# Kernel optimization log

Hardware: AMD Instinct MI355X
Metric: run time of the kernel (lower is better)

The kernel has to match this reference:

```python
import jax, jax.numpy as jnp
import numpy as np

B, LMAX, H, D = 128, 256, 16, 64
NEG_INF = -1e9  # finite mask value to keep padded softmax rows NaN-free


def _lengths():
    # deterministic varlen mix: 64 seqs of 128 tokens, 64 of 256 -> total 24576
    lens = np.array([128] * 64 + [256] * 64, dtype=np.int64)
    rng = np.random.default_rng(0)
    rng.shuffle(lens)
    return lens


def setup_inputs() -> dict:
    key = jax.random.key(0)
    lens = _lengths()
    cu = np.zeros(B + 1, dtype=np.int64)
    cu[1:] = np.cumsum(lens)
    T = int(cu[-1])  # 24576 packed tokens

    kq, kk, kv = jax.random.split(key, 3)
    q = jax.random.normal(kq, (T, H, D), dtype=jnp.float32)
    k = jax.random.normal(kk, (T, H, D), dtype=jnp.float32)
    v = jax.random.normal(kv, (T, H, D), dtype=jnp.float32)

    pos = np.arange(LMAX)[None, :]                      # [1, LMAX]
    mask = pos < lens[:, None]                          # [B, LMAX] valid-token mask
    gather_idx = np.where(mask, cu[:-1, None] + pos, 0).astype(np.int32)

    # packed token t -> flat padded index b*LMAX + (t - cu[b])
    b_of = np.repeat(np.arange(B), lens)
    inv_idx = (b_of * LMAX + (np.arange(T) - cu[b_of])).astype(np.int32)

    return {
        "q": q, "k": k, "v": v,
        "cu_seqlens_q": jnp.asarray(cu, dtype=jnp.int32),
        "cu_seqlens_k": jnp.asarray(cu, dtype=jnp.int32),
        "gather_idx": jnp.asarray(gather_idx),
        "mask": jnp.asarray(mask),
        "inv_idx": jnp.asarray(inv_idx),
        "max_seqlen_q": LMAX,
        "max_seqlen_k": LMAX,
    }


def reference(q, k, v, cu_seqlens_q, cu_seqlens_k, gather_idx, mask, inv_idx,
              max_seqlen_q, max_seqlen_k):
    # Pad packed [T,H,D] -> [B,L,H,D]; padded slots point at token 0 but are masked out.
    qp = q[gather_idx]  # [B, L, H, D]
    kp = k[gather_idx]
    vp = v[gather_idx]
    scale = 1.0 / jnp.sqrt(jnp.asarray(q.shape[-1], q.dtype))
    scores = jnp.einsum("bqhd,bkhd->bhqk", qp, kp) * scale  # [B, H, L, L]
    scores = jnp.where(mask[:, None, None, :], scores, NEG_INF)
    w = jax.nn.softmax(scores, axis=-1)
    out_p = jnp.einsum("bhqk,bkhd->bqhd", w, vp)            # [B, L, H, D]
    # Unpad back to packed layout [T, H, D]
    return out_p.reshape(-1, q.shape[1], q.shape[2])[inv_idx]
```

## Files before the change

kernel.cpp:

```cpp
#include <hip/hip_runtime.h>
#include <hip/hip_bf16.h>


using bf16x8 = __attribute__((ext_vector_type(8))) short;
using u16x8  = __attribute__((ext_vector_type(8))) unsigned short;
using f32x4  = __attribute__((ext_vector_type(4))) float;

#define MFMA(a, b, c) __builtin_amdgcn_mfma_f32_16x16x32_bf16((a), (b), (c), 0, 0, 0)

constexpr int H  = 16;
constexpr int D  = 64;
constexpr int RS = H * D;
constexpr float QSCALE = 0.125f * 1.44269504088896f;
constexpr float THR    = 11.5f;

__device__ inline unsigned short bfbits(float x) {
  return __builtin_bit_cast(unsigned short, __float2bfloat16(x));
}
__device__ inline float bff(unsigned short u) {
  unsigned v = ((unsigned)u) << 16;
  return __builtin_bit_cast(float, v);
}

__global__ __launch_bounds__(512, 4)
void fa_mfma4_kernel(const float* __restrict__ qg, const float* __restrict__ kg,
                     const float* __restrict__ vg, const int* __restrict__ cu,
                     float* __restrict__ outg) {
  __shared__ unsigned short kph[2][64 * 64];
  __shared__ unsigned short kpl[2][64 * 64];
  __shared__ unsigned short vth[2][64 * 64];

  const int bid   = (int)blockIdx.x;
  const int pp    = ((bid >> 4) << 3) + (bid & 7);
  const int chunk = (bid >> 3) & 1;
  const int b = pp >> 4, h = pp & 15;

  const int t0 = cu[b];
  const int L  = cu[b + 1] - t0;
  if (chunk * 128 >= L) return;
  const int nt = L >> 6;

  const int tid = (int)threadIdx.x, lane = tid & 63, w = tid >> 6;
  const int g = lane >> 4, qj = lane & 15;

  const int s_key = tid >> 3, s_d0 = (tid & 7) * 8;
  const int kidx  = s_key * 64 + (((s_d0 >> 3) ^ (s_key & 7)) << 3);
  const int s_vd  = tid & 63,  s_k0 = (tid >> 6) * 8;
  const int vidx  = s_vd * 64 + (((s_k0 >> 3) ^ (s_vd & 7)) << 3);

  const float* kbase = kg + (size_t)t0 * RS + h * D;
  const float* vbase = vg + (size_t)t0 * RS + h * D;

  bf16x8 qh[2], ql[2];
  {
    const float* qrow = qg + (size_t)(t0 + chunk * 128 + w * 16 + qj) * RS + h * D;
#pragma unroll
    for (int ks = 0; ks < 2; ++ks) {
      const float4 f0 = *reinterpret_cast<const float4*>(qrow + ks * 32 + g * 8);
      const float4 f1 = *reinterpret_cast<const float4*>(qrow + ks * 32 + g * 8 + 4);
      const float f[8] = {f0.x, f0.y, f0.z, f0.w, f1.x, f1.y, f1.z, f1.w};
#pragma unroll
      for (int j = 0; j < 8; ++j) {
        const float x = f[j] * QSCALE;
        const unsigned short hs = bfbits(x);
        qh[ks][j] = (short)hs;
        ql[ks][j] = (short)bfbits(x - bff(hs));
      }
    }
  }

  f32x4 acc[4];
#pragma unroll
  for (int n = 0; n < 4; ++n) acc[n] = (f32x4){0.f, 0.f, 0.f, 0.f};
  float m = -1e30f, lsum = 0.f;

  float4 ka, kb; float va[8];
  auto load_t = [&](int t) {
    const float* kr = kbase + (size_t)(t * 64 + s_key) * RS + s_d0;
    ka = *reinterpret_cast<const float4*>(kr);
    kb = *reinterpret_cast<const float4*>(kr + 4);
    const float* vp = vbase + (size_t)(t * 64 + s_k0) * RS + s_vd;
#pragma unroll
    for (int i = 0; i < 8; ++i) va[i] = vp[(size_t)i * RS];
  };
  auto cvt_write = [&](int buf) {
    u16x8 ch, cl, cv;
    const float kf[8] = {ka.x, ka.y, ka.z, ka.w, kb.x, kb.y, kb.z, kb.w};
#pragma unroll
    for (int i = 0; i < 8; ++i) {
      const unsigned short hs = bfbits(kf[i]);
      ch[i] = hs;
      cl[i] = bfbits(kf[i] - bff(hs));
    }
#pragma unroll
    for (int i = 0; i < 8; ++i) cv[i] = bfbits(va[i]);
    *reinterpret_cast<u16x8*>(&kph[buf][kidx]) = ch;
    *reinterpret_cast<u16x8*>(&kpl[buf][kidx]) = cl;
    *reinterpret_cast<u16x8*>(&vth[buf][vidx]) = cv;
  };

  auto compute = [&](int buf) {
    const unsigned short* KH = kph[buf];
    const unsigned short* KL = kpl[buf];
    const unsigned short* VT = vth[buf];
    f32x4 sc[4];
#pragma unroll
    for (int kt = 0; kt < 4; ++kt) sc[kt] = (f32x4){0.f, 0.f, 0.f, 0.f};
    __builtin_amdgcn_s_setprio(1);
#pragma unroll
    for (int kt = 0; kt < 4; ++kt) {
#pragma unroll
      for (int ks = 0; ks < 2; ++ks) {
        const int idx = (kt * 16 + qj) * 64 + (((ks * 4 + g) ^ (qj & 7)) << 3);
        const bf16x8 khi = *reinterpret_cast<const bf16x8*>(&KH[idx]);
        const bf16x8 klo = *reinterpret_cast<const bf16x8*>(&KL[idx]);
        sc[kt] = MFMA(khi, qh[ks], sc[kt]);
        sc[kt] = MFMA(klo, qh[ks], sc[kt]);
        sc[kt] = MFMA(khi, ql[ks], sc[kt]);
      }
    }
    __builtin_amdgcn_s_setprio(0);

    float tmax = sc[0][0];
#pragma unroll
    for (int kt = 0; kt < 4; ++kt)
#pragma unroll
      for (int r = 0; r < 4; ++r) tmax = fmaxf(tmax, sc[kt][r]);
    tmax = fmaxf(tmax, __shfl_xor(tmax, 16));
    tmax = fmaxf(tmax, __shfl_xor(tmax, 32));
    if (!__all(tmax <= m + THR)) {
      const float newm = fmaxf(m, tmax);
      const float corr = exp2f(m - newm);
      m = newm;
      lsum *= corr;
#pragma unroll
      for (int r = 0; r < 4; ++r) {
        const float cr = __shfl(corr, g * 4 + r);
#pragma unroll
        for (int n = 0; n < 4; ++n) acc[n][r] *= cr;
      }
    }
    float p[4][4], ps = 0.f;
#pragma unroll
    for (int kt = 0; kt < 4; ++kt)
#pragma unroll
      for (int r = 0; r < 4; ++r) {
        p[kt][r] = exp2f(sc[kt][r] - m);
        ps += p[kt][r];
      }
    ps += __shfl_xor(ps, 16);
    ps += __shfl_xor(ps, 32);
    lsum += ps;

#pragma unroll
    for (int c = 0; c < 2; ++c) {
      bf16x8 pah, pal;
#pragma unroll
      for (int j = 0; j < 8; ++j) {
        const int sl  = (((2 * g + (j >> 2)) & 3) << 4) + qj;
        const float fa = __shfl(p[2 * c][j & 3], sl);
        const float fb = __shfl(p[2 * c + 1][j & 3], sl);
        const float pv = (g & 2) ? fb : fa;
        const unsigned short hb = bfbits(pv);
        pah[j] = (short)hb;
        pal[j] = (short)bfbits(pv - bff(hb));
      }
      __builtin_amdgcn_s_setprio(1);
#pragma unroll
      for (int n = 0; n < 4; ++n) {
        const int idx = (n * 16 + qj) * 64 + (((4 * c + g) ^ (qj & 7)) << 3);
        const bf16x8 vh = *reinterpret_cast<const bf16x8*>(&VT[idx]);
        acc[n] = MFMA(pah, vh, acc[n]);
        acc[n] = MFMA(pal, vh, acc[n]);
      }
      __builtin_amdgcn_s_setprio(0);
    }
  };

  load_t(0);
  cvt_write(0);
  if (nt > 1) load_t(1);
  asm volatile("s_waitcnt lgkmcnt(0)" ::: "memory");
  __builtin_amdgcn_s_barrier();
  asm volatile("" ::: "memory");

  for (int t = 0; t < nt; ++t) {
    const int cur = t & 1;
    if (t + 1 < nt) {
      cvt_write(cur ^ 1);
      if (t + 2 < nt) load_t(t + 2);
    }
    compute(cur);
    if (t + 1 < nt) {
      asm volatile("s_waitcnt lgkmcnt(0)" ::: "memory");
      __builtin_amdgcn_s_barrier();
      asm volatile("" ::: "memory");
    }
  }

  const float linv = 1.0f / lsum;
#pragma unroll
  for (int r = 0; r < 4; ++r) {
    const float lr = __shfl(linv, g * 4 + r);
    const int qrow = chunk * 128 + w * 16 + g * 4 + r;
    float* op = outg + (size_t)(t0 + qrow) * RS + h * D + qj;
    op[0]  = acc[0][r] * lr;
    op[16] = acc[1][r] * lr;
    op[32] = acc[2][r] * lr;
    op[48] = acc[3][r] * lr;
  }
}

extern "C" void kernel_launch(void* const* d_in, const int* in_sizes, int n_in,
                              void* d_out, int out_size, void* d_ws, size_t ws_size,
                              hipStream_t stream) {
  (void)in_sizes; (void)n_in; (void)d_ws; (void)ws_size; (void)out_size;
  const float* q  = (const float*)d_in[0];
  const float* k  = (const float*)d_in[1];
  const float* v  = (const float*)d_in[2];
  const int*   cu = (const int*)d_in[3];
  float* out = (float*)d_out;

  fa_mfma4_kernel<<<dim3(4096), dim3(512), 0, stream>>>(q, k, v, cu, out);
}
```

Before: 124.4 us.

## Switch attention to 32x32x16 MFMA tiles with 4 waves per block

Replaces the 16x16x32 bf16 MFMA tiling with 32x32x16 MFMAs, so each wave owns 32 query rows and blocks shrink from 8 to 4 waves. The K/V staging loads now pull 16 elements per thread. The P-matrix repacking moves from many per-element shuffles to a half-wave xor exchange of packed bf16 pairs, and row-wise correction factors go through shared memory. The goal is fewer MFMA issues, less shuffle overhead and more reuse per LDS read, at the cost of more registers per thread and lower occupancy.

```diff
diff --git a/kernel.cpp b/kernel.cpp
--- a/kernel.cpp
+++ b/kernel.cpp
@@ -4,9 +4,10 @@
 
 using bf16x8 = __attribute__((ext_vector_type(8))) short;
 using u16x8  = __attribute__((ext_vector_type(8))) unsigned short;
-using f32x4  = __attribute__((ext_vector_type(4))) float;
-
-#define MFMA(a, b, c) __builtin_amdgcn_mfma_f32_16x16x32_bf16((a), (b), (c), 0, 0, 0)
+using u32x4  = __attribute__((ext_vector_type(4))) unsigned;
+using f32x16 = __attribute__((ext_vector_type(16))) float;
+
+#define MFMA32(a, b, c) __builtin_amdgcn_mfma_f32_32x32x16_bf16((a), (b), (c), 0, 0, 0)
 
 constexpr int H  = 16;
 constexpr int D  = 64;
@@ -21,14 +22,18 @@
   unsigned v = ((unsigned)u) << 16;
   return __builtin_bit_cast(float, v);
 }
-
-__global__ __launch_bounds__(512, 4)
-void fa_mfma4_kernel(const float* __restrict__ qg, const float* __restrict__ kg,
+__device__ inline unsigned pack2(float x, float y) {
+  return (unsigned)bfbits(x) | ((unsigned)bfbits(y) << 16);
+}
+
+__global__ __launch_bounds__(256, 3)
+void fa_mfma7_kernel(const float* __restrict__ qg, const float* __restrict__ kg,
                      const float* __restrict__ vg, const int* __restrict__ cu,
                      float* __restrict__ outg) {
   __shared__ unsigned short kph[2][64 * 64];
   __shared__ unsigned short kpl[2][64 * 64];
   __shared__ unsigned short vth[2][64 * 64];
+  __shared__ float lsc[4 * 32];
 
   const int bid   = (int)blockIdx.x;
   const int pp    = ((bid >> 4) << 3) + (bid & 7);
@@ -41,23 +46,27 @@
   const int nt = L >> 6;
 
   const int tid = (int)threadIdx.x, lane = tid & 63, w = tid >> 6;
-  const int g = lane >> 4, qj = lane & 15;
-
-  const int s_key = tid >> 3, s_d0 = (tid & 7) * 8;
-  const int kidx  = s_key * 64 + (((s_d0 >> 3) ^ (s_key & 7)) << 3);
-  const int s_vd  = tid & 63,  s_k0 = (tid >> 6) * 8;
-  const int vidx  = s_vd * 64 + (((s_k0 >> 3) ^ (s_vd & 7)) << 3);
+  const int hi = lane >> 5, qj = lane & 31;
+  const int qbase = chunk * 128 + w * 32;
+
+  const int k_key = tid >> 2, kd0 = (tid & 3) * 16;
+  const int kidx0 = k_key * 64 + ((((kd0 >> 3) + 0) ^ (k_key & 7)) << 3);
+  const int kidx1 = k_key * 64 + ((((kd0 >> 3) + 1) ^ (k_key & 7)) << 3);
+  const int v_d = tid & 63, vk0 = (tid >> 6) * 16;
+  const int vidx0 = v_d * 64 + ((((vk0 >> 3) + 0) ^ (v_d & 7)) << 3);
+  const int vidx1 = v_d * 64 + ((((vk0 >> 3) + 1) ^ (v_d & 7)) << 3);
 
   const float* kbase = kg + (size_t)t0 * RS + h * D;
   const float* vbase = vg + (size_t)t0 * RS + h * D;
 
-  bf16x8 qh[2], ql[2];
+  bf16x8 qh[4], ql[4];
   {
-    const float* qrow = qg + (size_t)(t0 + chunk * 128 + w * 16 + qj) * RS + h * D;
-#pragma unroll
-    for (int ks = 0; ks < 2; ++ks) {
-      const float4 f0 = *reinterpret_cast<const float4*>(qrow + ks * 32 + g * 8);
-      const float4 f1 = *reinterpret_cast<const float4*>(qrow + ks * 32 + g * 8 + 4);
+    const float* qrow = qg + (size_t)(t0 + qbase + qj) * RS + h * D;
+#pragma unroll
+    for (int ks = 0; ks < 4; ++ks) {
+      const int d0 = ks * 16 + hi * 8;
+      const float4 f0 = *reinterpret_cast<const float4*>(qrow + d0);
+      const float4 f1 = *reinterpret_cast<const float4*>(qrow + d0 + 4);
       const float f[8] = {f0.x, f0.y, f0.z, f0.w, f1.x, f1.y, f1.z, f1.w};
 #pragma unroll
       for (int j = 0; j < 8; ++j) {
@@ -69,109 +78,144 @@
     }
   }
 
-  f32x4 acc[4];
-#pragma unroll
-  for (int n = 0; n < 4; ++n) acc[n] = (f32x4){0.f, 0.f, 0.f, 0.f};
+  f32x16 acc0, acc1;
+#pragma unroll
+  for (int r = 0; r < 16; ++r) { acc0[r] = 0.f; acc1[r] = 0.f; }
   float m = -1e30f, lsum = 0.f;
 
-  float4 ka, kb; float va[8];
+  float kf[16], vf[16];
   auto load_t = [&](int t) {
-    const float* kr = kbase + (size_t)(t * 64 + s_key) * RS + s_d0;
-    ka = *reinterpret_cast<const float4*>(kr);
-    kb = *reinterpret_cast<const float4*>(kr + 4);
-    const float* vp = vbase + (size_t)(t * 64 + s_k0) * RS + s_vd;
-#pragma unroll
-    for (int i = 0; i < 8; ++i) va[i] = vp[(size_t)i * RS];
+    const float* kr = kbase + (size_t)(t * 64 + k_key) * RS + kd0;
+#pragma unroll
+    for (int i = 0; i < 16; i += 4) {
+      const float4 f4 = *reinterpret_cast<const float4*>(kr + i);
+      kf[i] = f4.x; kf[i + 1] = f4.y; kf[i + 2] = f4.z; kf[i + 3] = f4.w;
+    }
+    const float* vp = vbase + (size_t)(t * 64 + vk0) * RS + v_d;
+#pragma unroll
+    for (int i = 0; i < 16; ++i) vf[i] = vp[(size_t)i * RS];
   };
   auto cvt_write = [&](int buf) {
-    u16x8 ch, cl, cv;
-    const float kf[8] = {ka.x, ka.y, ka.z, ka.w, kb.x, kb.y, kb.z, kb.w};
+    u16x8 h0, h1, l0, l1, v0, v1;
 #pragma unroll
     for (int i = 0; i < 8; ++i) {
-      const unsigned short hs = bfbits(kf[i]);
-      ch[i] = hs;
-      cl[i] = bfbits(kf[i] - bff(hs));
-    }
-#pragma unroll
-    for (int i = 0; i < 8; ++i) cv[i] = bfbits(va[i]);
-    *reinterpret_cast<u16x8*>(&kph[buf][kidx]) = ch;
-    *reinterpret_cast<u16x8*>(&kpl[buf][kidx]) = cl;
-    *reinterpret_cast<u16x8*>(&vth[buf][vidx]) = cv;
+      const unsigned short a = bfbits(kf[i]), c = bfbits(kf[8 + i]);
+      h0[i] = a; l0[i] = bfbits(kf[i] - bff(a));
+      h1[i] = c; l1[i] = bfbits(kf[8 + i] - bff(c));
+      v0[i] = bfbits(vf[i]);
+      v1[i] = bfbits(vf[8 + i]);
+    }
+    *reinterpret_cast<u16x8*>(&kph[buf][kidx0]) = h0;
+    *reinterpret_cast<u16x8*>(&kph[buf][kidx1]) = h1;
+    *reinterpret_cast<u16x8*>(&kpl[buf][kidx0]) = l0;
+    *reinterpret_cast<u16x8*>(&kpl[buf][kidx1]) = l1;
+    *reinterpret_cast<u16x8*>(&vth[buf][vidx0]) = v0;
+    *reinterpret_cast<u16x8*>(&vth[buf][vidx1]) = v1;
+  };
+
+  const bool hib = (hi != 0);
+  auto mix4 = [&](unsigned a0, unsigned a1, unsigned a2, unsigned a3) -> u32x4 {
+    const unsigned t02 = hib ? a0 : a2;
+    const unsigned t13 = hib ? a1 : a3;
+    const unsigned c02 = (unsigned)__shfl_xor((int)t02, 32);
+    const unsigned c13 = (unsigned)__shfl_xor((int)t13, 32);
+    u32x4 r;
+    r[0] = hib ? c02 : a0;
+    r[1] = hib ? c13 : a1;
+    r[2] = hib ? a2 : c02;
+    r[3] = hib ? a3 : c13;
+    return r;
+  };
+  auto build_pa = [&](const float* x, bf16x8& pah, bf16x8& pal) {
+    pah = __builtin_bit_cast(bf16x8,
+        mix4(pack2(x[0], x[1]), pack2(x[2], x[3]),
+             pack2(x[4], x[5]), pack2(x[6], x[7])));
+    float y[8];
+#pragma unroll
+    for (int i = 0; i < 8; ++i) y[i] = x[i] - bff(bfbits(x[i]));
+    pal = __builtin_bit_cast(bf16x8,
+        mix4(pack2(y[0], y[1]), pack2(y[2], y[3]),
+             pack2(y[4], y[5]), pack2(y[6], y[7])));
   };
 
   auto compute = [&](int buf) {
     const unsigned short* KH = kph[buf];
     const unsigned short* KL = kpl[buf];
     const unsigned short* VT = vth[buf];
-    f32x4 sc[4];
-#pragma unroll
-    for (int kt = 0; kt < 4; ++kt) sc[kt] = (f32x4){0.f, 0.f, 0.f, 0.f};
+    f32x16 sc0, sc1;
+#pragma unroll
+    for (int r = 0; r < 16; ++r) { sc0[r] = 0.f; sc1[r] = 0.f; }
     __builtin_amdgcn_s_setprio(1);
 #pragma unroll
-    for (int kt = 0; kt < 4; ++kt) {
-#pragma unroll
-      for (int ks = 0; ks < 2; ++ks) {
-        const int idx = (kt * 16 + qj) * 64 + (((ks * 4 + g) ^ (qj & 7)) << 3);
+    for (int kt = 0; kt < 2; ++kt) {
+#pragma unroll
+      for (int ks = 0; ks < 4; ++ks) {
+        const int idx = (kt * 32 + qj) * 64 + (((ks * 2 + hi) ^ (qj & 7)) << 3);
         const bf16x8 khi = *reinterpret_cast<const bf16x8*>(&KH[idx]);
         const bf16x8 klo = *reinterpret_cast<const bf16x8*>(&KL[idx]);
-        sc[kt] = MFMA(khi, qh[ks], sc[kt]);
-        sc[kt] = MFMA(klo, qh[ks], sc[kt]);
-        sc[kt] = MFMA(khi, ql[ks], sc[kt]);
+        if (kt == 0) {
+          sc0 = MFMA32(khi, qh[ks], sc0);
+          sc0 = MFMA32(klo, qh[ks], sc0);
+          sc0 = MFMA32(khi, ql[ks], sc0);
+        } else {
+          sc1 = MFMA32(khi, qh[ks], sc1);
+          sc1 = MFMA32(klo, qh[ks], sc1);
+          sc1 = MFMA32(khi, ql[ks], sc1);
+        }
       }
     }
     __builtin_amdgcn_s_setprio(0);
 
-    float tmax = sc[0][0];
-#pragma unroll
-    for (int kt = 0; kt < 4; ++kt)
-#pragma unroll
-      for (int r = 0; r < 4; ++r) tmax = fmaxf(tmax, sc[kt][r]);
-    tmax = fmaxf(tmax, __shfl_xor(tmax, 16));
+    float tmax = sc0[0];
+#pragma unroll
+    for (int r = 1; r < 16; ++r) tmax = fmaxf(tmax, sc0[r]);
+#pragma unroll
+    for (int r = 0; r < 16; ++r) tmax = fmaxf(tmax, sc1[r]);
     tmax = fmaxf(tmax, __shfl_xor(tmax, 32));
     if (!__all(tmax <= m + THR)) {
       const float newm = fmaxf(m, tmax);
       const float corr = exp2f(m - newm);
       m = newm;
       lsum *= corr;
-#pragma unroll
-      for (int r = 0; r < 4; ++r) {
-        const float cr = __shfl(corr, g * 4 + r);
-#pragma unroll
-        for (int n = 0; n < 4; ++n) acc[n][r] *= cr;
-      }
-    }
-    float p[4][4], ps = 0.f;
-#pragma unroll
-    for (int kt = 0; kt < 4; ++kt)
-#pragma unroll
-      for (int r = 0; r < 4; ++r) {
-        p[kt][r] = exp2f(sc[kt][r] - m);
-        ps += p[kt][r];
-      }
-    ps += __shfl_xor(ps, 16);
-    ps += __shfl_xor(ps, 32);
-    lsum += ps;
-
-#pragma unroll
-    for (int c = 0; c < 2; ++c) {
+      if (hi == 0) lsc[w * 32 + qj] = corr;
+      __builtin_amdgcn_wave_barrier();
+#pragma unroll
+      for (int r = 0; r < 16; ++r) {
+        const float c = lsc[w * 32 + ((r & 3) + 8 * (r >> 2) + 4 * hi)];
+        acc0[r] *= c; acc1[r] *= c;
+      }
+    }
+    float ps = 0.f;
+#pragma unroll
+    for (int r = 0; r < 16; ++r) {
+      sc0[r] = exp2f(sc0[r] - m); ps += sc0[r];
+    }
+#pragma unroll
+    for (int r = 0; r < 16; ++r) {
+      sc1[r] = exp2f(sc1[r] - m); ps += sc1[r];
+    }
+    lsum += ps + __shfl_xor(ps, 32);
+
+#pragma unroll
+    for (int ks2 = 0; ks2 < 4; ++ks2) {
+      float px[8];
+#pragma unroll
+      for (int i = 0; i < 8; ++i)
+        px[i] = (ks2 & 2) ? sc1[(ks2 & 1) * 8 + i] : sc0[(ks2 & 1) * 8 + i];
       bf16x8 pah, pal;
-#pragma unroll
-      for (int j = 0; j < 8; ++j) {
-        const int sl  = (((2 * g + (j >> 2)) & 3) << 4) + qj;
-        const float fa = __shfl(p[2 * c][j & 3], sl);
-        const float fb = __shfl(p[2 * c + 1][j & 3], sl);
-        const float pv = (g & 2) ? fb : fa;
-        const unsigned short hb = bfbits(pv);
-        pah[j] = (short)hb;
-        pal[j] = (short)bfbits(pv - bff(hb));
-      }
+      build_pa(px, pah, pal);
       __builtin_amdgcn_s_setprio(1);
 #pragma unroll
-      for (int n = 0; n < 4; ++n) {
-        const int idx = (n * 16 + qj) * 64 + (((4 * c + g) ^ (qj & 7)) << 3);
+      for (int n = 0; n < 2; ++n) {
+        const int idx = (n * 32 + qj) * 64 + (((ks2 * 2 + hi) ^ (qj & 7)) << 3);
         const bf16x8 vh = *reinterpret_cast<const bf16x8*>(&VT[idx]);
-        acc[n] = MFMA(pah, vh, acc[n]);
-        acc[n] = MFMA(pal, vh, acc[n]);
+        if (n == 0) {
+          acc0 = MFMA32(pah, vh, acc0);
+          acc0 = MFMA32(pal, vh, acc0);
+        } else {
+          acc1 = MFMA32(pah, vh, acc1);
+          acc1 = MFMA32(pal, vh, acc1);
+        }
       }
       __builtin_amdgcn_s_setprio(0);
     }
@@ -198,16 +242,15 @@
     }
   }
 
-  const float linv = 1.0f / lsum;
-#pragma unroll
-  for (int r = 0; r < 4; ++r) {
-    const float lr = __shfl(linv, g * 4 + r);
-    const int qrow = chunk * 128 + w * 16 + g * 4 + r;
-    float* op = outg + (size_t)(t0 + qrow) * RS + h * D + qj;
-    op[0]  = acc[0][r] * lr;
-    op[16] = acc[1][r] * lr;
-    op[32] = acc[2][r] * lr;
-    op[48] = acc[3][r] * lr;
+  if (hi == 0) lsc[w * 32 + qj] = 1.0f / lsum;
+  __builtin_amdgcn_wave_barrier();
+#pragma unroll
+  for (int r = 0; r < 16; ++r) {
+    const int row = (r & 3) + 8 * (r >> 2) + 4 * hi;
+    const float li = lsc[w * 32 + row];
+    float* op = outg + (size_t)(t0 + qbase + row) * RS + h * D + qj;
+    op[0]  = acc0[r] * li;
+    op[32] = acc1[r] * li;
   }
 }
 
@@ -221,5 +264,5 @@
   const int*   cu = (const int*)d_in[3];
   float* out = (float*)d_out;
 
-  fa_mfma4_kernel<<<dim3(4096), dim3(512), 0, stream>>>(q, k, v, cu, out);
-}
+  fa_mfma7_kernel<<<dim3(4096), dim3(256), 0, stream>>>(q, k, v, cu, out);
+}
```

Result: slower. 127.5 us (+2.5%).
